# Kernel tuning notes

Hardware: AMD Instinct MI355X
Metric: run time of the kernel (lower is better)

Reference implementation:

```python
import jax, jax.numpy as jnp
import numpy as np


def setup_inputs() -> dict:
    key = jax.random.key(0)
    k1, k2 = jax.random.split(key)
    B, T, D = 16, 4096, 1024
    hidden_states = jax.random.normal(k1, (B, T, D), dtype=jnp.float32)
    mask = jnp.ones((B, T), dtype=jnp.int32)
    context_vector = jax.random.normal(k2, (D,), dtype=jnp.float32)
    return {"hidden_states": hidden_states, "mask": mask, "context_vector": context_vector}


def reference(hidden_states, mask, context_vector):
    # scores: (B, T) dot of each token with learned context vector
    scores = jnp.einsum("btd,d->bt", hidden_states, context_vector)
    scores = jnp.where(mask == 0, -jnp.inf, scores)
    attn_weights = jax.nn.softmax(scores, axis=-1)  # (B, T)
    pooled = jnp.einsum("bt,btd->bd", attn_weights, hidden_states)
    return pooled
```

## Files before the change

### kernel.cpp

```cpp
#include <hip/hip_runtime.h>
#include <math.h>


__global__ __launch_bounds__(256) void ap_partial(
    const float* __restrict__ hs, const int* __restrict__ mask,
    const float* __restrict__ ctx,
    float* __restrict__ accs, float* __restrict__ ms, float* __restrict__ ls,
    int T, int blocksPerB, int tokensPerWave)
{
    const int D = 1024;
    int bi    = blockIdx.x;
    int b     = bi / blocksPerB;
    int chunk = bi - b * blocksPerB;
    int wave  = threadIdx.x >> 6;
    int lane  = threadIdx.x & 63;

    int t0 = chunk * (tokensPerWave * 4) + wave * tokensPerWave;

    const float4* ctx4 = (const float4*)ctx;
    float4 c0 = ctx4[0 * 64 + lane];
    float4 c1 = ctx4[1 * 64 + lane];
    float4 c2 = ctx4[2 * 64 + lane];
    float4 c3 = ctx4[3 * 64 + lane];

    float4 a0 = {0.f,0.f,0.f,0.f}, a1 = {0.f,0.f,0.f,0.f};
    float4 a2 = {0.f,0.f,0.f,0.f}, a3 = {0.f,0.f,0.f,0.f};
    float m = -INFINITY, l = 0.0f;

    const float4* hp = (const float4*)hs + ((size_t)b * T + t0) * (D / 4);
    const int*    mp = mask + (size_t)b * T + t0;

    for (int i = 0; i < tokensPerWave; ++i) {
        const float4* row = hp + (size_t)i * (D / 4);
        float4 h0 = row[0 * 64 + lane];
        float4 h1 = row[1 * 64 + lane];
        float4 h2 = row[2 * 64 + lane];
        float4 h3 = row[3 * 64 + lane];

        float p = 0.0f;
        p = fmaf(h0.x, c0.x, p); p = fmaf(h0.y, c0.y, p);
        p = fmaf(h0.z, c0.z, p); p = fmaf(h0.w, c0.w, p);
        p = fmaf(h1.x, c1.x, p); p = fmaf(h1.y, c1.y, p);
        p = fmaf(h1.z, c1.z, p); p = fmaf(h1.w, c1.w, p);
        p = fmaf(h2.x, c2.x, p); p = fmaf(h2.y, c2.y, p);
        p = fmaf(h2.z, c2.z, p); p = fmaf(h2.w, c2.w, p);
        p = fmaf(h3.x, c3.x, p); p = fmaf(h3.y, c3.y, p);
        p = fmaf(h3.z, c3.z, p); p = fmaf(h3.w, c3.w, p);

        #pragma unroll
        for (int off = 32; off > 0; off >>= 1) p += __shfl_xor(p, off);

        if (mp[i] != 0) {
            float mn = fmaxf(m, p);
            float c  = __expf(m - mn);
            float w  = __expf(p - mn);
            l = fmaf(l, c, w);
            a0.x = fmaf(a0.x, c, w * h0.x); a0.y = fmaf(a0.y, c, w * h0.y);
            a0.z = fmaf(a0.z, c, w * h0.z); a0.w = fmaf(a0.w, c, w * h0.w);
            a1.x = fmaf(a1.x, c, w * h1.x); a1.y = fmaf(a1.y, c, w * h1.y);
            a1.z = fmaf(a1.z, c, w * h1.z); a1.w = fmaf(a1.w, c, w * h1.w);
            a2.x = fmaf(a2.x, c, w * h2.x); a2.y = fmaf(a2.y, c, w * h2.y);
            a2.z = fmaf(a2.z, c, w * h2.z); a2.w = fmaf(a2.w, c, w * h2.w);
            a3.x = fmaf(a3.x, c, w * h3.x); a3.y = fmaf(a3.y, c, w * h3.y);
            a3.z = fmaf(a3.z, c, w * h3.z); a3.w = fmaf(a3.w, c, w * h3.w);
            m = mn;
        }
    }

    __shared__ float  s_m[4];
    __shared__ float  s_lf[4];
    __shared__ float4 s_acc[4][256];

    if (lane == 0) s_m[wave] = m;
    __syncthreads();
    float M = fmaxf(fmaxf(s_m[0], s_m[1]), fmaxf(s_m[2], s_m[3]));
    float f = (m == -INFINITY) ? 0.0f : __expf(m - M);
    if (lane == 0) s_lf[wave] = l * f;
    float4 t;
    t.x = a0.x * f; t.y = a0.y * f; t.z = a0.z * f; t.w = a0.w * f; s_acc[wave][0 * 64 + lane] = t;
    t.x = a1.x * f; t.y = a1.y * f; t.z = a1.z * f; t.w = a1.w * f; s_acc[wave][1 * 64 + lane] = t;
    t.x = a2.x * f; t.y = a2.y * f; t.z = a2.z * f; t.w = a2.w * f; s_acc[wave][2 * 64 + lane] = t;
    t.x = a3.x * f; t.y = a3.y * f; t.z = a3.z * f; t.w = a3.w * f; s_acc[wave][3 * 64 + lane] = t;
    __syncthreads();

    int tid = threadIdx.x;
    float4 v0 = s_acc[0][tid], v1 = s_acc[1][tid], v2 = s_acc[2][tid], v3 = s_acc[3][tid];
    float4 r;
    r.x = (v0.x + v1.x) + (v2.x + v3.x);
    r.y = (v0.y + v1.y) + (v2.y + v3.y);
    r.z = (v0.z + v1.z) + (v2.z + v3.z);
    r.w = (v0.w + v1.w) + (v2.w + v3.w);

    float4* accs4 = (float4*)(accs + (size_t)bi * D);
    accs4[tid] = r;
    if (tid == 0) {
        ms[bi] = M;
        ls[bi] = (s_lf[0] + s_lf[1]) + (s_lf[2] + s_lf[3]);
    }
}

__global__ __launch_bounds__(256) void ap_combine(
    const float* __restrict__ accs, const float* __restrict__ ms,
    const float* __restrict__ ls, float* __restrict__ out, int numChunks)
{
    int b   = blockIdx.x;
    int tid = threadIdx.x;
    const float* mB = ms + (size_t)b * numChunks;
    const float* lB = ls + (size_t)b * numChunks;

    float M = -INFINITY;
    for (int c = 0; c < numChunks; ++c) M = fmaxf(M, mB[c]);
    float L = 0.0f;
    for (int c = 0; c < numChunks; ++c) {
        float mc = mB[c];
        float f  = (mc == -INFINITY) ? 0.0f : __expf(mc - M);
        L += lB[c] * f;
    }

    float rx = 0.f, ry = 0.f, rz = 0.f, rw = 0.f;
    const float4* accs4 = (const float4*)accs;
    for (int c = 0; c < numChunks; ++c) {
        float mc = mB[c];
        float f  = (mc == -INFINITY) ? 0.0f : __expf(mc - M);
        float4 v = accs4[((size_t)b * numChunks + c) * 256 + tid];
        rx = fmaf(v.x, f, rx); ry = fmaf(v.y, f, ry);
        rz = fmaf(v.z, f, rz); rw = fmaf(v.w, f, rw);
    }
    float inv = 1.0f / L;
    float4 o; o.x = rx * inv; o.y = ry * inv; o.z = rz * inv; o.w = rw * inv;
    ((float4*)out)[(size_t)b * 256 + tid] = o;
}

extern "C" void kernel_launch(void* const* d_in, const int* in_sizes, int n_in,
                              void* d_out, int out_size, void* d_ws, size_t ws_size,
                              hipStream_t stream)
{
    const float* hs   = (const float*)d_in[0];
    const int*   mask = (const int*)d_in[1];
    const float* ctx  = (const float*)d_in[2];

    const int D = 1024;
    int B = out_size / D;
    int T = in_sizes[1] / B;

    int blocksPerB = 64;
    while (blocksPerB > 1 &&
           ((T % (4 * blocksPerB)) != 0 ||
            (size_t)B * blocksPerB * (size_t)(D + 2) * sizeof(float) > ws_size))
        blocksPerB >>= 1;
    int tokensPerWave = T / (4 * blocksPerB);
    int numP = B * blocksPerB;

    float* accs = (float*)d_ws;
    float* ms   = accs + (size_t)numP * D;
    float* ls   = ms + numP;

    ap_partial<<<numP, 256, 0, stream>>>(hs, mask, ctx, accs, ms, ls,
                                         T, blocksPerB, tokensPerWave);
    ap_combine<<<B, 256, 0, stream>>>(accs, ms, ls, (float*)d_out, blocksPerB);
}
```

Before: 387.7 us.

## Fuse combine into partial kernel via last-block atomic counter, add nontemporal loads

Merges the partial and combine kernels into one launch: each block bumps a per-batch atomic counter, and the last block to finish for a batch performs the cross-chunk softmax merge and writes the output. A memset clears the counters first. Hidden-state loads become nontemporal, and the online softmax rescales only when the running max grows. This trades one kernel launch for a memset, fences and atomics, and leaves a tail where a single block per batch does the combine.

```diff
diff --git a/kernel.cpp b/kernel.cpp
--- a/kernel.cpp
+++ b/kernel.cpp
@@ -2,10 +2,13 @@
 #include <math.h>
 
 
-__global__ __launch_bounds__(256) void ap_partial(
+typedef float f32x4 __attribute__((ext_vector_type(4)));
+
+__global__ __launch_bounds__(256) void ap_fused(
     const float* __restrict__ hs, const int* __restrict__ mask,
     const float* __restrict__ ctx,
     float* __restrict__ accs, float* __restrict__ ms, float* __restrict__ ls,
+    int* __restrict__ counters, float* __restrict__ out,
     int T, int blocksPerB, int tokensPerWave)
 {
     const int D = 1024;
@@ -14,28 +17,29 @@
     int chunk = bi - b * blocksPerB;
     int wave  = threadIdx.x >> 6;
     int lane  = threadIdx.x & 63;
+    int tid   = threadIdx.x;
 
     int t0 = chunk * (tokensPerWave * 4) + wave * tokensPerWave;
 
-    const float4* ctx4 = (const float4*)ctx;
-    float4 c0 = ctx4[0 * 64 + lane];
-    float4 c1 = ctx4[1 * 64 + lane];
-    float4 c2 = ctx4[2 * 64 + lane];
-    float4 c3 = ctx4[3 * 64 + lane];
+    const f32x4* ctx4 = (const f32x4*)ctx;
+    f32x4 c0 = ctx4[0 * 64 + lane];
+    f32x4 c1 = ctx4[1 * 64 + lane];
+    f32x4 c2 = ctx4[2 * 64 + lane];
+    f32x4 c3 = ctx4[3 * 64 + lane];
 
-    float4 a0 = {0.f,0.f,0.f,0.f}, a1 = {0.f,0.f,0.f,0.f};
-    float4 a2 = {0.f,0.f,0.f,0.f}, a3 = {0.f,0.f,0.f,0.f};
+    f32x4 a0 = {0.f,0.f,0.f,0.f}, a1 = {0.f,0.f,0.f,0.f};
+    f32x4 a2 = {0.f,0.f,0.f,0.f}, a3 = {0.f,0.f,0.f,0.f};
     float m = -INFINITY, l = 0.0f;
 
-    const float4* hp = (const float4*)hs + ((size_t)b * T + t0) * (D / 4);
-    const int*    mp = mask + (size_t)b * T + t0;
+    const f32x4* hp = (const f32x4*)hs + ((size_t)b * T + t0) * (D / 4);
+    const int*   mp = mask + (size_t)b * T + t0;
 
     for (int i = 0; i < tokensPerWave; ++i) {
-        const float4* row = hp + (size_t)i * (D / 4);
-        float4 h0 = row[0 * 64 + lane];
-        float4 h1 = row[1 * 64 + lane];
-        float4 h2 = row[2 * 64 + lane];
-        float4 h3 = row[3 * 64 + lane];
+        const f32x4* row = hp + (size_t)i * (D / 4);
+        f32x4 h0 = __builtin_nontemporal_load(&row[0 * 64 + lane]);
+        f32x4 h1 = __builtin_nontemporal_load(&row[1 * 64 + lane]);
+        f32x4 h2 = __builtin_nontemporal_load(&row[2 * 64 + lane]);
+        f32x4 h3 = __builtin_nontemporal_load(&row[3 * 64 + lane]);
 
         float p = 0.0f;
         p = fmaf(h0.x, c0.x, p); p = fmaf(h0.y, c0.y, p);
@@ -51,84 +55,84 @@
         for (int off = 32; off > 0; off >>= 1) p += __shfl_xor(p, off);
 
         if (mp[i] != 0) {
-            float mn = fmaxf(m, p);
-            float c  = __expf(m - mn);
-            float w  = __expf(p - mn);
-            l = fmaf(l, c, w);
-            a0.x = fmaf(a0.x, c, w * h0.x); a0.y = fmaf(a0.y, c, w * h0.y);
-            a0.z = fmaf(a0.z, c, w * h0.z); a0.w = fmaf(a0.w, c, w * h0.w);
-            a1.x = fmaf(a1.x, c, w * h1.x); a1.y = fmaf(a1.y, c, w * h1.y);
-            a1.z = fmaf(a1.z, c, w * h1.z); a1.w = fmaf(a1.w, c, w * h1.w);
-            a2.x = fmaf(a2.x, c, w * h2.x); a2.y = fmaf(a2.y, c, w * h2.y);
-            a2.z = fmaf(a2.z, c, w * h2.z); a2.w = fmaf(a2.w, c, w * h2.w);
-            a3.x = fmaf(a3.x, c, w * h3.x); a3.y = fmaf(a3.y, c, w * h3.y);
-            a3.z = fmaf(a3.z, c, w * h3.z); a3.w = fmaf(a3.w, c, w * h3.w);
-            m = mn;
+            if (p > m) {
+                float c = __expf(m - p);
+                l *= c;
+                a0 *= c; a1 *= c; a2 *= c; a3 *= c;
+                m = p;
+            }
+            float w = __expf(p - m);
+            l += w;
+            a0.x = fmaf(w, h0.x, a0.x); a0.y = fmaf(w, h0.y, a0.y);
+            a0.z = fmaf(w, h0.z, a0.z); a0.w = fmaf(w, h0.w, a0.w);
+            a1.x = fmaf(w, h1.x, a1.x); a1.y = fmaf(w, h1.y, a1.y);
+            a1.z = fmaf(w, h1.z, a1.z); a1.w = fmaf(w, h1.w, a1.w);
+            a2.x = fmaf(w, h2.x, a2.x); a2.y = fmaf(w, h2.y, a2.y);
+            a2.z = fmaf(w, h2.z, a2.z); a2.w = fmaf(w, h2.w, a2.w);
+            a3.x = fmaf(w, h3.x, a3.x); a3.y = fmaf(w, h3.y, a3.y);
+            a3.z = fmaf(w, h3.z, a3.z); a3.w = fmaf(w, h3.w, a3.w);
         }
     }
 
-    __shared__ float  s_m[4];
-    __shared__ float  s_lf[4];
-    __shared__ float4 s_acc[4][256];
+    __shared__ float s_m[4];
+    __shared__ float s_lf[4];
+    __shared__ f32x4 s_acc[4][256];
+    __shared__ int   s_last;
 
     if (lane == 0) s_m[wave] = m;
     __syncthreads();
     float M = fmaxf(fmaxf(s_m[0], s_m[1]), fmaxf(s_m[2], s_m[3]));
     float f = (m == -INFINITY) ? 0.0f : __expf(m - M);
     if (lane == 0) s_lf[wave] = l * f;
-    float4 t;
-    t.x = a0.x * f; t.y = a0.y * f; t.z = a0.z * f; t.w = a0.w * f; s_acc[wave][0 * 64 + lane] = t;
-    t.x = a1.x * f; t.y = a1.y * f; t.z = a1.z * f; t.w = a1.w * f; s_acc[wave][1 * 64 + lane] = t;
-    t.x = a2.x * f; t.y = a2.y * f; t.z = a2.z * f; t.w = a2.w * f; s_acc[wave][2 * 64 + lane] = t;
-    t.x = a3.x * f; t.y = a3.y * f; t.z = a3.z * f; t.w = a3.w * f; s_acc[wave][3 * 64 + lane] = t;
+    s_acc[wave][0 * 64 + lane] = a0 * f;
+    s_acc[wave][1 * 64 + lane] = a1 * f;
+    s_acc[wave][2 * 64 + lane] = a2 * f;
+    s_acc[wave][3 * 64 + lane] = a3 * f;
     __syncthreads();
 
-    int tid = threadIdx.x;
-    float4 v0 = s_acc[0][tid], v1 = s_acc[1][tid], v2 = s_acc[2][tid], v3 = s_acc[3][tid];
-    float4 r;
-    r.x = (v0.x + v1.x) + (v2.x + v3.x);
-    r.y = (v0.y + v1.y) + (v2.y + v3.y);
-    r.z = (v0.z + v1.z) + (v2.z + v3.z);
-    r.w = (v0.w + v1.w) + (v2.w + v3.w);
+    f32x4 v0 = s_acc[0][tid], v1 = s_acc[1][tid], v2 = s_acc[2][tid], v3 = s_acc[3][tid];
+    f32x4 r = (v0 + v1) + (v2 + v3);
 
-    float4* accs4 = (float4*)(accs + (size_t)bi * D);
+    f32x4* accs4 = (f32x4*)(accs + (size_t)bi * D);
     accs4[tid] = r;
     if (tid == 0) {
         ms[bi] = M;
         ls[bi] = (s_lf[0] + s_lf[1]) + (s_lf[2] + s_lf[3]);
     }
-}
 
-__global__ __launch_bounds__(256) void ap_combine(
-    const float* __restrict__ accs, const float* __restrict__ ms,
-    const float* __restrict__ ls, float* __restrict__ out, int numChunks)
-{
-    int b   = blockIdx.x;
-    int tid = threadIdx.x;
-    const float* mB = ms + (size_t)b * numChunks;
-    const float* lB = ls + (size_t)b * numChunks;
+    __threadfence();
+    __syncthreads();
+    if (tid == 0) {
+        int old = atomicAdd(&counters[b], 1);
+        s_last = (old == blocksPerB - 1) ? 1 : 0;
+    }
+    __syncthreads();
+    if (!s_last) return;
+    __threadfence();
 
-    float M = -INFINITY;
-    for (int c = 0; c < numChunks; ++c) M = fmaxf(M, mB[c]);
-    float L = 0.0f;
-    for (int c = 0; c < numChunks; ++c) {
+    const float* mB = ms + (size_t)b * blocksPerB;
+    const float* lB = ls + (size_t)b * blocksPerB;
+
+    float M2 = -INFINITY;
+    for (int c = 0; c < blocksPerB; ++c) M2 = fmaxf(M2, mB[c]);
+    float L2 = 0.0f;
+    for (int c = 0; c < blocksPerB; ++c) {
         float mc = mB[c];
-        float f  = (mc == -INFINITY) ? 0.0f : __expf(mc - M);
-        L += lB[c] * f;
+        float fc = (mc == -INFINITY) ? 0.0f : __expf(mc - M2);
+        L2 += lB[c] * fc;
     }
 
-    float rx = 0.f, ry = 0.f, rz = 0.f, rw = 0.f;
-    const float4* accs4 = (const float4*)accs;
-    for (int c = 0; c < numChunks; ++c) {
+    f32x4 racc = {0.f,0.f,0.f,0.f};
+    const f32x4* allAccs4 = (const f32x4*)accs;
+    for (int c = 0; c < blocksPerB; ++c) {
         float mc = mB[c];
-        float f  = (mc == -INFINITY) ? 0.0f : __expf(mc - M);
-        float4 v = accs4[((size_t)b * numChunks + c) * 256 + tid];
-        rx = fmaf(v.x, f, rx); ry = fmaf(v.y, f, ry);
-        rz = fmaf(v.z, f, rz); rw = fmaf(v.w, f, rw);
+        float fc = (mc == -INFINITY) ? 0.0f : __expf(mc - M2);
+        f32x4 v = allAccs4[((size_t)b * blocksPerB + c) * 256 + tid];
+        racc.x = fmaf(v.x, fc, racc.x); racc.y = fmaf(v.y, fc, racc.y);
+        racc.z = fmaf(v.z, fc, racc.z); racc.w = fmaf(v.w, fc, racc.w);
     }
-    float inv = 1.0f / L;
-    float4 o; o.x = rx * inv; o.y = ry * inv; o.z = rz * inv; o.w = rw * inv;
-    ((float4*)out)[(size_t)b * 256 + tid] = o;
+    float inv = 1.0f / L2;
+    ((f32x4*)out)[(size_t)b * 256 + tid] = racc * inv;
 }
 
 extern "C" void kernel_launch(void* const* d_in, const int* in_sizes, int n_in,
@@ -146,16 +150,18 @@
     int blocksPerB = 64;
     while (blocksPerB > 1 &&
            ((T % (4 * blocksPerB)) != 0 ||
-            (size_t)B * blocksPerB * (size_t)(D + 2) * sizeof(float) > ws_size))
+            256 + (size_t)B * blocksPerB * (size_t)(D + 2) * sizeof(float) > ws_size))
         blocksPerB >>= 1;
     int tokensPerWave = T / (4 * blocksPerB);
     int numP = B * blocksPerB;
 
-    float* accs = (float*)d_ws;
-    float* ms   = accs + (size_t)numP * D;
-    float* ls   = ms + numP;
+    int*   counters = (int*)d_ws;
+    float* accs     = (float*)((char*)d_ws + 256);
+    float* ms       = accs + (size_t)numP * D;
+    float* ls       = ms + numP;
 
-    ap_partial<<<numP, 256, 0, stream>>>(hs, mask, ctx, accs, ms, ls,
-                                         T, blocksPerB, tokensPerWave);
-    ap_combine<<<B, 256, 0, stream>>>(accs, ms, ls, (float*)d_out, blocksPerB);
+    (void)hipMemsetAsync(counters, 0, 256, stream);
+    ap_fused<<<numP, 256, 0, stream>>>(hs, mask, ctx, accs, ms, ls,
+                                       counters, (float*)d_out,
+                                       T, blocksPerB, tokensPerWave);
 }
```

New measurement: 524.5 us. 35.3% more time.
